# Performance work log

Measured on AMD Instinct MI355X. Metric: run time of the kernel, lower is better.

The kernel has to match this reference:

```python
import jax, jax.numpy as jnp
import numpy as np

BS, NQ, NC, NT = 16, 900, 91, 1600
COST_CLASS, COST_BBOX, COST_GIOU = 1.0, 5.0, 2.0


def box_cxcywh_to_xyxy(b):
    cx, cy, w, h = b[..., 0], b[..., 1], b[..., 2], b[..., 3]
    return jnp.stack([cx - 0.5 * w, cy - 0.5 * h, cx + 0.5 * w, cy + 0.5 * h], axis=-1)


def generalized_box_iou(boxes1, boxes2):
    # boxes1: [N,4] xyxy, boxes2: [M,4] xyxy -> [N,M]
    area1 = (boxes1[:, 2] - boxes1[:, 0]) * (boxes1[:, 3] - boxes1[:, 1])  # [N]
    area2 = (boxes2[:, 2] - boxes2[:, 0]) * (boxes2[:, 3] - boxes2[:, 1])  # [M]
    lt = jnp.maximum(boxes1[:, None, :2], boxes2[None, :, :2])  # [N,M,2]
    rb = jnp.minimum(boxes1[:, None, 2:], boxes2[None, :, 2:])  # [N,M,2]
    wh = jnp.clip(rb - lt, 0.0)
    inter = wh[..., 0] * wh[..., 1]  # [N,M]
    union = area1[:, None] + area2[None, :] - inter
    iou = inter / union
    # smallest enclosing box
    lt_c = jnp.minimum(boxes1[:, None, :2], boxes2[None, :, :2])
    rb_c = jnp.maximum(boxes1[:, None, 2:], boxes2[None, :, 2:])
    wh_c = jnp.clip(rb_c - lt_c, 0.0)
    area_c = wh_c[..., 0] * wh_c[..., 1]
    return iou - (area_c - union) / area_c


def setup_inputs() -> dict:
    key = jax.random.key(0)
    k1, k2, k3, k4 = jax.random.split(key, 4)
    pred_logits = jax.random.normal(k1, (BS, NQ, NC), dtype=jnp.float32)
    # cxcywh in (0,1): guarantee positive w,h and sane boxes
    pred_boxes = jax.random.uniform(k2, (BS, NQ, 4), dtype=jnp.float32, minval=0.05, maxval=0.95)
    tgt_bbox = jax.random.uniform(k3, (NT, 4), dtype=jnp.float32, minval=0.05, maxval=0.95)
    tgt_ids = jax.random.randint(k4, (NT,), 0, NC, dtype=jnp.int32)
    return {"pred_logits": pred_logits, "pred_boxes": pred_boxes,
            "tgt_bbox": tgt_bbox, "tgt_ids": tgt_ids}


def reference(pred_logits, pred_boxes, tgt_bbox, tgt_ids):
    bs, num_queries = pred_logits.shape[:2]
    out_prob = jax.nn.softmax(pred_logits.reshape(-1, pred_logits.shape[-1]), axis=-1)  # [bs*nq, NC]
    out_bbox = pred_boxes.reshape(-1, 4)  # [bs*nq, 4]
    cost_class = -out_prob[:, tgt_ids]  # [bs*nq, NT]
    # L1 cdist
    cost_bbox = jnp.sum(jnp.abs(out_bbox[:, None, :] - tgt_bbox[None, :, :]), axis=-1)
    cost_giou = -generalized_box_iou(box_cxcywh_to_xyxy(out_bbox), box_cxcywh_to_xyxy(tgt_bbox))
    C = COST_BBOX * cost_bbox + COST_CLASS * cost_class + COST_GIOU * cost_giou
    return C.reshape(bs, num_queries, -1)
```

## Files before the change

### kernel.cpp

```cpp
#include <hip/hip_runtime.h>
#include <math.h>

#define BS_ 16
#define NQ_ 900
#define NC_ 91
#define NT_ 1600
#define NROWS_ (BS_ * NQ_)
#define TILE_R 4
#define TPB 320
#define NBLK (NROWS_ / TILE_R)
#define KITER (NT_ / TPB)

__global__ __launch_bounds__(TPB) void matcher_cost_kernel(
    const float* __restrict__ logits,
    const float* __restrict__ pboxes,
    const float4* __restrict__ tboxes,
    const int*   __restrict__ tids,
    float* __restrict__ out)
{
    const int base = blockIdx.x * TILE_R;
    const int tid  = threadIdx.x;
    const int lane = tid & 63;
    const int wave = tid >> 6;

    __shared__ __align__(16) float sneg[NC_ * TILE_R];

    if (wave < TILE_R) {
        const float* lrow = logits + (base + wave) * NC_;
        float v0 = lrow[lane];
        float v1 = (lane < NC_ - 64) ? lrow[64 + lane] : -INFINITY;
        float m = fmaxf(v0, v1);
        #pragma unroll
        for (int off = 32; off >= 1; off >>= 1)
            m = fmaxf(m, __shfl_xor(m, off, 64));
        float e0 = __expf(v0 - m);
        float e1 = (lane < NC_ - 64) ? __expf(v1 - m) : 0.0f;
        float s = e0 + e1;
        #pragma unroll
        for (int off = 32; off >= 1; off >>= 1)
            s += __shfl_xor(s, off, 64);
        const float inv_s = __builtin_amdgcn_rcpf(s);
        sneg[lane * TILE_R + wave] = fmaf(-e0, inv_s, 2.0f);
        if (lane < NC_ - 64)
            sneg[(64 + lane) * TILE_R + wave] = fmaf(-e1, inv_s, 2.0f);
    }

    float4 tb[KITER];
    int    id[KITER];
    #pragma unroll
    for (int k = 0; k < KITER; ++k) {
        const int j = k * TPB + tid;
        tb[k] = tboxes[j];
        id[k] = tids[j];
    }

    float qcx[TILE_R], qcy[TILE_R], qw[TILE_R], qh[TILE_R];
    float qx0[TILE_R], qy0[TILE_R], qx1[TILE_R], qy1[TILE_R], qarea[TILE_R];
    #pragma unroll
    for (int r = 0; r < TILE_R; ++r) {
        const float4 qb = *reinterpret_cast<const float4*>(pboxes + (base + r) * 4);
        qcx[r] = qb.x; qcy[r] = qb.y; qw[r] = qb.z; qh[r] = qb.w;
        qx0[r] = fmaf(-0.5f, qb.z, qb.x);
        qy0[r] = fmaf(-0.5f, qb.w, qb.y);
        qx1[r] = fmaf( 0.5f, qb.z, qb.x);
        qy1[r] = fmaf( 0.5f, qb.w, qb.y);
        qarea[r] = qb.z * qb.w;
    }

    __syncthreads();

    float4 pp[KITER];
    #pragma unroll
    for (int k = 0; k < KITER; ++k)
        pp[k] = *reinterpret_cast<const float4*>(&sneg[id[k] * TILE_R]);

    #pragma unroll
    for (int k = 0; k < KITER; ++k) {
        const int j = k * TPB + tid;
        const float4 t = tb[k];
        const float tx0 = fmaf(-0.5f, t.z, t.x);
        const float ty0 = fmaf(-0.5f, t.w, t.y);
        const float tx1 = fmaf( 0.5f, t.z, t.x);
        const float ty1 = fmaf( 0.5f, t.w, t.y);
        const float tarea = t.z * t.w;
        const float p[TILE_R] = {pp[k].x, pp[k].y, pp[k].z, pp[k].w};

        #pragma unroll
        for (int r = 0; r < TILE_R; ++r) {
            const float cb = fabsf(qcx[r] - t.x) + fabsf(qcy[r] - t.y)
                           + fabsf(qw[r]  - t.z) + fabsf(qh[r]  - t.w);

            const float dx = fminf(qx1[r], tx1) - fmaxf(qx0[r], tx0);
            const float dy = fminf(qy1[r], ty1) - fmaxf(qy0[r], ty0);
            const float inter = fmaxf(dx, 0.0f) * fmaxf(dy, 0.0f);
            const float uni   = (qarea[r] + tarea) - inter;

            const float cw = (qw[r] + t.z) - dx;
            const float ch = (qh[r] + t.w) - dy;
            const float areac = cw * ch;

            float c = fmaf(5.0f, cb, p[r]);
            c = fmaf(-2.0f * inter, __builtin_amdgcn_rcpf(uni),   c);
            c = fmaf(-2.0f * uni,   __builtin_amdgcn_rcpf(areac), c);

            __builtin_nontemporal_store(c, out + (base + r) * NT_ + j);
        }
    }
}

extern "C" void kernel_launch(void* const* d_in, const int* in_sizes, int n_in,
                              void* d_out, int out_size, void* d_ws, size_t ws_size,
                              hipStream_t stream) {
    const float*  logits = (const float*)d_in[0];
    const float*  pboxes = (const float*)d_in[1];
    const float4* tboxes = (const float4*)d_in[2];
    const int*    tids   = (const int*)d_in[3];
    float* out = (float*)d_out;

    matcher_cost_kernel<<<NBLK, TPB, 0, stream>>>(logits, pboxes, tboxes, tids, out);
}
```

Measured before the change: 118.9 us.

## Remap threads to row-by-4-column tiles with float4 stores and packed float2 math

```diff
diff --git a/kernel.cpp b/kernel.cpp
--- a/kernel.cpp
+++ b/kernel.cpp
@@ -9,19 +9,23 @@
 #define TILE_R 4
 #define TPB 320
 #define NBLK (NROWS_ / TILE_R)
-#define KITER (NT_ / TPB)
+#define KITER 5
+
+typedef float f2 __attribute__((ext_vector_type(2)));
 
 __global__ __launch_bounds__(TPB) void matcher_cost_kernel(
     const float* __restrict__ logits,
-    const float* __restrict__ pboxes,
+    const float4* __restrict__ pboxes,
     const float4* __restrict__ tboxes,
-    const int*   __restrict__ tids,
-    float* __restrict__ out)
+    const int4*  __restrict__ tids4,
+    float4* __restrict__ out4)
 {
     const int base = blockIdx.x * TILE_R;
     const int tid  = threadIdx.x;
     const int lane = tid & 63;
     const int wave = tid >> 6;
+    const int r    = tid & 3;
+    const int c4b  = tid >> 2;
 
     __shared__ __align__(16) float sneg[NC_ * TILE_R];
 
@@ -45,66 +49,67 @@
             sneg[(64 + lane) * TILE_R + wave] = fmaf(-e1, inv_s, 2.0f);
     }
 
-    float4 tb[KITER];
-    int    id[KITER];
-    #pragma unroll
-    for (int k = 0; k < KITER; ++k) {
-        const int j = k * TPB + tid;
-        tb[k] = tboxes[j];
-        id[k] = tids[j];
-    }
-
-    float qcx[TILE_R], qcy[TILE_R], qw[TILE_R], qh[TILE_R];
-    float qx0[TILE_R], qy0[TILE_R], qx1[TILE_R], qy1[TILE_R], qarea[TILE_R];
-    #pragma unroll
-    for (int r = 0; r < TILE_R; ++r) {
-        const float4 qb = *reinterpret_cast<const float4*>(pboxes + (base + r) * 4);
-        qcx[r] = qb.x; qcy[r] = qb.y; qw[r] = qb.z; qh[r] = qb.w;
-        qx0[r] = fmaf(-0.5f, qb.z, qb.x);
-        qy0[r] = fmaf(-0.5f, qb.w, qb.y);
-        qx1[r] = fmaf( 0.5f, qb.z, qb.x);
-        qy1[r] = fmaf( 0.5f, qb.w, qb.y);
-        qarea[r] = qb.z * qb.w;
-    }
+    const float4 qb = pboxes[base + r];
+    const f2 qc  = {qb.x, qb.y};
+    const f2 qwh = {qb.z, qb.w};
+    const f2 q0  = qc - 0.5f * qwh;
+    const f2 q1  = qc + 0.5f * qwh;
+    const float qarea = qb.z * qb.w;
+    const int orow = (base + r) * (NT_ / 4);
 
     __syncthreads();
 
-    float4 pp[KITER];
-    #pragma unroll
-    for (int k = 0; k < KITER; ++k)
-        pp[k] = *reinterpret_cast<const float4*>(&sneg[id[k] * TILE_R]);
-
     #pragma unroll
     for (int k = 0; k < KITER; ++k) {
-        const int j = k * TPB + tid;
-        const float4 t = tb[k];
-        const float tx0 = fmaf(-0.5f, t.z, t.x);
-        const float ty0 = fmaf(-0.5f, t.w, t.y);
-        const float tx1 = fmaf( 0.5f, t.z, t.x);
-        const float ty1 = fmaf( 0.5f, t.w, t.y);
-        const float tarea = t.z * t.w;
-        const float p[TILE_R] = {pp[k].x, pp[k].y, pp[k].z, pp[k].w};
+        const int c4 = c4b + 80 * k;
+        const int j0 = c4 * 4;
 
+        const int4 id4 = tids4[c4];
+        const float4 b0 = tboxes[j0 + 0];
+        const float4 b1 = tboxes[j0 + 1];
+        const float4 b2 = tboxes[j0 + 2];
+        const float4 b3 = tboxes[j0 + 3];
+
+        const float p0 = sneg[id4.x * TILE_R + r];
+        const float p1 = sneg[id4.y * TILE_R + r];
+        const float p2 = sneg[id4.z * TILE_R + r];
+        const float p3 = sneg[id4.w * TILE_R + r];
+
+        float4 res;
+        const float4 bb[4] = {b0, b1, b2, b3};
+        const float  pp[4] = {p0, p1, p2, p3};
+        float rr[4];
         #pragma unroll
-        for (int r = 0; r < TILE_R; ++r) {
-            const float cb = fabsf(qcx[r] - t.x) + fabsf(qcy[r] - t.y)
-                           + fabsf(qw[r]  - t.z) + fabsf(qh[r]  - t.w);
+        for (int i = 0; i < 4; ++i) {
+            const float4 b = bb[i];
+            const f2 tc  = {b.x, b.y};
+            const f2 twh = {b.z, b.w};
+            const f2 t0  = tc - 0.5f * twh;
+            const f2 t1  = tc + 0.5f * twh;
+            const float ta = b.z * b.w;
 
-            const float dx = fminf(qx1[r], tx1) - fmaxf(qx0[r], tx0);
-            const float dy = fminf(qy1[r], ty1) - fmaxf(qy0[r], ty0);
-            const float inter = fmaxf(dx, 0.0f) * fmaxf(dy, 0.0f);
-            const float uni   = (qarea[r] + tarea) - inter;
+            const f2 dc  = qc - tc;
+            const f2 dwh = qwh - twh;
+            const float cb = (fabsf(dc.x) + fabsf(dc.y))
+                           + (fabsf(dwh.x) + fabsf(dwh.y));
 
-            const float cw = (qw[r] + t.z) - dx;
-            const float ch = (qh[r] + t.w) - dy;
-            const float areac = cw * ch;
+            const f2 mn = __builtin_elementwise_min(q1, t1);
+            const f2 mx = __builtin_elementwise_max(q0, t0);
+            const f2 d  = mn - mx;
+            const f2 z  = __builtin_elementwise_max(d, (f2){0.0f, 0.0f});
+            const float inter = z.x * z.y;
+            const float uni   = (qarea + ta) - inter;
 
-            float c = fmaf(5.0f, cb, p[r]);
+            const f2 cwh = (qwh + twh) - d;
+            const float areac = cwh.x * cwh.y;
+
+            float c = fmaf(5.0f, cb, pp[i]);
             c = fmaf(-2.0f * inter, __builtin_amdgcn_rcpf(uni),   c);
             c = fmaf(-2.0f * uni,   __builtin_amdgcn_rcpf(areac), c);
-
-            __builtin_nontemporal_store(c, out + (base + r) * NT_ + j);
+            rr[i] = c;
         }
+        res.x = rr[0]; res.y = rr[1]; res.z = rr[2]; res.w = rr[3];
+        out4[orow + c4] = res;
     }
 }
 
@@ -112,10 +117,10 @@
                               void* d_out, int out_size, void* d_ws, size_t ws_size,
                               hipStream_t stream) {
     const float*  logits = (const float*)d_in[0];
-    const float*  pboxes = (const float*)d_in[1];
+    const float4* pboxes = (const float4*)d_in[1];
     const float4* tboxes = (const float4*)d_in[2];
-    const int*    tids   = (const int*)d_in[3];
-    float* out = (float*)d_out;
+    const int4*   tids4  = (const int4*)d_in[3];
+    float4* out4 = (float4*)d_out;
 
-    matcher_cost_kernel<<<NBLK, TPB, 0, stream>>>(logits, pboxes, tboxes, tids, out);
+    matcher_cost_kernel<<<NBLK, TPB, 0, stream>>>(logits, pboxes, tboxes, tids4, out4);
 }
```

New measurement: 121.3 us. No clear change (+2.0%).
